# Kernel tuning notes

Measured on AMD Instinct MI355X. Metric: run time of the kernel, lower is better.

## Reference

```python
import jax, jax.numpy as jnp
import numpy as np

B, CIN, COUT, K, H, W = 2, 128, 64, 64, 128, 128
BN_EPS = 1e-5


def setup_inputs() -> dict:
    key = jax.random.key(0)
    k1, k2, k3, k4 = jax.random.split(key, 4)
    x = jax.random.normal(k1, (B, CIN, H, W), dtype=jnp.float32)
    index = jax.random.randint(k2, (B, 1, H, W), 0, K)  # superpixel labels
    # kaiming_uniform(a=sqrt(5)) ~ uniform with bound sqrt(6/((1+5)*fan_in)) = 1/sqrt(fan_in)
    Wft = jax.random.uniform(k3, (CIN, COUT), dtype=jnp.float32,
                             minval=-1.0, maxval=1.0) / np.sqrt(CIN).astype(np.float32)
    Wm = jax.random.uniform(k4, (COUT, COUT), dtype=jnp.float32,
                            minval=-1.0, maxval=1.0) / np.sqrt(COUT).astype(np.float32)
    gamma = jnp.ones((COUT,), jnp.float32)
    beta = jnp.zeros((COUT,), jnp.float32)
    return {"x": x, "index": index, "Wft": Wft, "Wm": Wm, "gamma": gamma, "beta": beta}


def _gnn_forward(x, index, Wft, Wm, gamma, beta):
    # FeatureTransform: [B,Cin,H,W] -> [B,Cout,H,W]
    xt = jnp.einsum('bchw,co->bohw', x, Wft)

    idx = index[:, 0]                                   # [B,H,W]
    oh = jax.nn.one_hot(idx, K, dtype=xt.dtype)         # [B,H,W,K]

    # RegionalMeans (segment-mean over superpixels; equivalent to the
    # repeated-tensor multiply+sum in the torch code, without the 5D blowup)
    block_sum = oh.sum(axis=(1, 2))                     # [B,K]
    sums = jnp.einsum('bhwk,bohw->bko', oh, xt)         # [B,K,Cout]
    denom = block_sum + (block_sum == 0).astype(xt.dtype)
    means = sums / denom[..., None]                     # [B,K,Cout]

    # Adj: pairwise Mahalanobis distance with learned cov = Wm @ Wm.T
    cov = Wm @ Wm.T
    inv_cov = jnp.linalg.inv(cov)
    diff = means[:, :, None, :] - means[:, None, :, :]  # [B,K,K,Cout]
    q = jnp.einsum('bijc,cd,bijd->bij', diff, inv_cov, diff)
    dist = jnp.sqrt(jnp.maximum(q, 1e-12))              # clamp: diagonal q==0
    adj = jnp.exp(-dist)                                # [B,K,K]

    # GCN propagate: adjacency-weighted aggregation of region means
    adj_means = jnp.einsum('bij,bjo->bio', adj, means)  # [B,K,Cout]

    # sum_k one_hot_k * (x_rep + adj_means_k) == xt + gather(adj_means, idx)
    gathered = jnp.take_along_axis(adj_means, idx.reshape(B, -1, 1), axis=1)
    gathered = gathered.reshape(B, H, W, COUT).transpose(0, 3, 1, 2)
    features = jax.nn.relu(xt + gathered)               # [B,Cout,H,W]

    # BatchNorm2d (training-mode batch statistics, biased variance)
    mean = features.mean(axis=(0, 2, 3), keepdims=True)
    var = features.var(axis=(0, 2, 3), keepdims=True)
    out = (features - mean) / jnp.sqrt(var + BN_EPS)
    out = out * gamma[None, :, None, None] + beta[None, :, None, None]
    return out


def reference(x, index, Wft, Wm, gamma, beta):
    return _gnn_forward(x, index, Wft, Wm, gamma, beta)
```

## Files before the change

### kernel.cpp

```cpp
#include <hip/hip_runtime.h>
#include <hip/hip_bf16.h>

#define CIN   128
#define COUT  64
#define HW    16384

typedef __hip_bfloat16 bf16;

#define OFF_XT    0u
#define OFF_PS    1048576u
#define OFF_PC    2097152u
#define OFF_MEANS 2129920u
#define OFF_DIAG  2138112u
#define OFF_INV   2138240u
#define OFF_ADJM  2142336u
#define OFF_BNP   2150528u

__device__ __forceinline__ unsigned short f2bfu(float f) {
  union { bf16 h; unsigned short u; } cv; cv.h = __float2bfloat16(f); return cv.u;
}
__device__ __forceinline__ float bf2f(unsigned short u) {
  union { unsigned int i; float f; } cv; cv.i = ((unsigned int)u) << 16; return cv.f;
}

__global__ __launch_bounds__(256, 2) void k1_xt_bins_inv(
    const float* __restrict__ x, const int* __restrict__ index,
    const float* __restrict__ Wft, const float* __restrict__ Wm,
    float* __restrict__ ws)
{
  __shared__ __align__(16) float smem[16384];
  const int blk = blockIdx.x, tid = threadIdx.x;
  if (blk != 0) {
    float* xl = smem;
    float* wl = smem + 8192;
    const int eb = blk - 1;
    const int b = eb >> 8, ps = eb & 255;
    const float* xg = x + (size_t)b * CIN * HW + ps * 64;
#pragma unroll
    for (int j = 0; j < 8; ++j) {
      const int fj = j * 256 + tid;
      const int c = fj >> 4, q4 = (fj & 15) * 4;
      *(float4*)&xl[c * 64 + q4] = *(const float4*)(xg + (size_t)c * HW + q4);
      *(float4*)&wl[c * 64 + q4] = *(const float4*)(Wft + c * 64 + q4);
    }
    __syncthreads();
    const int px_grp = tid & 15, o_grp = tid >> 4;
    const int px = ps * 64 + px_grp * 4, o0 = o_grp * 4;
    float acc[16];
#pragma unroll
    for (int j = 0; j < 16; ++j) acc[j] = 0.f;
#pragma unroll 8
    for (int c = 0; c < 128; ++c) {
      const float4 xv = *(const float4*)&xl[c * 64 + px_grp * 4];
      const float4 wv = *(const float4*)&wl[c * 64 + o0];
      acc[ 0]=fmaf(xv.x,wv.x,acc[ 0]); acc[ 1]=fmaf(xv.y,wv.x,acc[ 1]);
      acc[ 2]=fmaf(xv.z,wv.x,acc[ 2]); acc[ 3]=fmaf(xv.w,wv.x,acc[ 3]);
      acc[ 4]=fmaf(xv.x,wv.y,acc[ 4]); acc[ 5]=fmaf(xv.y,wv.y,acc[ 5]);
      acc[ 6]=fmaf(xv.z,wv.y,acc[ 6]); acc[ 7]=fmaf(xv.w,wv.y,acc[ 7]);
      acc[ 8]=fmaf(xv.x,wv.z,acc[ 8]); acc[ 9]=fmaf(xv.y,wv.z,acc[ 9]);
      acc[10]=fmaf(xv.z,wv.z,acc[10]); acc[11]=fmaf(xv.w,wv.z,acc[11]);
      acc[12]=fmaf(xv.x,wv.w,acc[12]); acc[13]=fmaf(xv.y,wv.w,acc[13]);
      acc[14]=fmaf(xv.z,wv.w,acc[14]); acc[15]=fmaf(xv.w,wv.w,acc[15]);
    }
    unsigned short* xtu = (unsigned short*)(ws + OFF_XT);
#pragma unroll
    for (int oj = 0; oj < 4; ++oj) {
      ushort4 u;
      u.x = f2bfu(acc[oj*4+0]); u.y = f2bfu(acc[oj*4+1]);
      u.z = f2bfu(acc[oj*4+2]); u.w = f2bfu(acc[oj*4+3]);
      *(ushort4*)(xtu + (size_t)(b * 64 + o0 + oj) * HW + px) = u;
    }
    const int4 kv = *(const int4*)(index + b * HW + px);
    const int kk[4] = {kv.x, kv.y, kv.z, kv.w};
    __syncthreads();
    float* bins = smem;
    float* cnt  = smem + 64 * 68;
    for (int i = tid; i < 64 * 68 + 64; i += 256) smem[i] = 0.f;
    __syncthreads();
#pragma unroll
    for (int pj = 0; pj < 4; ++pj) {
      const int kb = kk[pj] * 68 + o0;
      atomicAdd(&bins[kb    ], acc[ 0 + pj]);
      atomicAdd(&bins[kb + 1], acc[ 4 + pj]);
      atomicAdd(&bins[kb + 2], acc[ 8 + pj]);
      atomicAdd(&bins[kb + 3], acc[12 + pj]);
    }
    if (o_grp == 0) {
#pragma unroll
      for (int pj = 0; pj < 4; ++pj) atomicAdd(&cnt[kk[pj]], 1.f);
    }
    __syncthreads();
    unsigned short* pb = (unsigned short*)(ws + OFF_PS) + (size_t)eb * 4096;
    {
      const int k = tid >> 2, ob = (tid & 3) * 16;
#pragma unroll
      for (int q = 0; q < 4; ++q) {
        const float4 v = *(const float4*)&bins[k * 68 + ob + q * 4];
        ushort4 u;
        u.x = f2bfu(v.x); u.y = f2bfu(v.y); u.z = f2bfu(v.z); u.w = f2bfu(v.w);
        *(ushort4*)(pb + k * 64 + ob + q * 4) = u;
      }
    }
    if (tid < 64) ws[OFF_PC + (size_t)(b * 64 + tid) * 256 + ps] = cnt[tid];
  } else {
    float* wm = smem;
    float* Rb = smem + 8192;
    float* Cb = smem + 8704;
    for (int e = tid; e < 4096; e += 256) wm[(e >> 6) * 68 + (e & 63)] = Wm[e];
    __syncthreads();
    const int ig = tid >> 4, jg = tid & 15;
    const int i0 = ig << 2, j0 = jg << 2;
    float c4[16];
#pragma unroll
    for (int q = 0; q < 16; ++q) c4[q] = 0.f;
    for (int cq = 0; cq < 64; cq += 4) {
      float4 a[4], bb[4];
#pragma unroll
      for (int ii = 0; ii < 4; ++ii) a[ii]  = *(const float4*)&wm[(i0+ii)*68 + cq];
#pragma unroll
      for (int jj = 0; jj < 4; ++jj) bb[jj] = *(const float4*)&wm[(j0+jj)*68 + cq];
#pragma unroll
      for (int ii = 0; ii < 4; ++ii)
#pragma unroll
        for (int jj = 0; jj < 4; ++jj)
          c4[ii*4+jj] = fmaf(a[ii].x, bb[jj].x, fmaf(a[ii].y, bb[jj].y,
                        fmaf(a[ii].z, bb[jj].z, fmaf(a[ii].w, bb[jj].w, c4[ii*4+jj]))));
    }
    __syncthreads();
    __builtin_amdgcn_s_setprio(3);
    int buf = 0;
#pragma unroll 1
    for (int p = 0; p < 16; ++p) {
      const int P = p << 2;
      float* Rp = Rb + buf * 256;
      float* Cp = Cb + buf * 256;
      if (ig == p) {
#pragma unroll
        for (int r = 0; r < 4; ++r) {
          float4 t; t.x = c4[r*4+0]; t.y = c4[r*4+1]; t.z = c4[r*4+2]; t.w = c4[r*4+3];
          *(float4*)&Rp[r * 64 + j0] = t;
        }
      }
      if (jg == p) {
#pragma unroll
        for (int ii = 0; ii < 4; ++ii) {
          float4 t; t.x = c4[ii*4+0]; t.y = c4[ii*4+1]; t.z = c4[ii*4+2]; t.w = c4[ii*4+3];
          *(float4*)&Cp[(i0 + ii) * 4] = t;
        }
      }
      __syncthreads();
      float dd[16];
#pragma unroll
      for (int r = 0; r < 4; ++r) *(float4*)&dd[r * 4] = *(const float4*)&Rp[r * 64 + P];
#pragma unroll
      for (int k = 0; k < 4; ++k) {
        const float rp = __builtin_amdgcn_rcpf(dd[k * 4 + k]);
        float ai[4], s[4];
#pragma unroll
        for (int j = 0; j < 4; ++j) s[j] = dd[k * 4 + j];
#pragma unroll
        for (int i = 0; i < 4; ++i) ai[i] = (i == k) ? (rp - 1.0f) : (-dd[i * 4 + k] * rp);
#pragma unroll
        for (int i = 0; i < 4; ++i)
#pragma unroll
          for (int j = 0; j < 4; ++j) dd[i * 4 + j] = fmaf(ai[i], s[j], dd[i * 4 + j]);
#pragma unroll
        for (int i = 0; i < 4; ++i) dd[i * 4 + k] = (i == k) ? rp : ai[i];
      }
      if (ig == p && jg == p) {
#pragma unroll
        for (int q = 0; q < 16; ++q) c4[q] = dd[q];
      } else if (ig == p) {
        float nr[16];
#pragma unroll
        for (int r = 0; r < 4; ++r)
#pragma unroll
          for (int jj = 0; jj < 4; ++jj) {
            float t = dd[r*4+0] * c4[0*4+jj];
            t = fmaf(dd[r*4+1], c4[1*4+jj], t);
            t = fmaf(dd[r*4+2], c4[2*4+jj], t);
            t = fmaf(dd[r*4+3], c4[3*4+jj], t);
            nr[r*4+jj] = t;
          }
#pragma unroll
        for (int q = 0; q < 16; ++q) c4[q] = nr[q];
      } else if (jg == p) {
        float nr[16];
#pragma unroll
        for (int ii = 0; ii < 4; ++ii)
#pragma unroll
          for (int cidx = 0; cidx < 4; ++cidx) {
            float t = c4[ii*4+0] * dd[0*4+cidx];
            t = fmaf(c4[ii*4+1], dd[1*4+cidx], t);
            t = fmaf(c4[ii*4+2], dd[2*4+cidx], t);
            t = fmaf(c4[ii*4+3], dd[3*4+cidx], t);
            nr[ii*4+cidx] = t;
          }
#pragma unroll
        for (int q = 0; q < 16; ++q) c4[q] = -nr[q];
      } else {
        float T[16];
#pragma unroll
        for (int ii = 0; ii < 4; ++ii) {
          const float4 ccv = *(const float4*)&Cp[(i0 + ii) * 4];
#pragma unroll
          for (int cidx = 0; cidx < 4; ++cidx) {
            float t = ccv.x * dd[0*4+cidx];
            t = fmaf(ccv.y, dd[1*4+cidx], t);
            t = fmaf(ccv.z, dd[2*4+cidx], t);
            t = fmaf(ccv.w, dd[3*4+cidx], t);
            T[ii*4+cidx] = t;
          }
        }
#pragma unroll
        for (int r = 0; r < 4; ++r) {
          const float4 rrv = *(const float4*)&Rp[r * 64 + j0];
#pragma unroll
          for (int ii = 0; ii < 4; ++ii) {
            c4[ii*4+0] = fmaf(-T[ii*4+r], rrv.x, c4[ii*4+0]);
            c4[ii*4+1] = fmaf(-T[ii*4+r], rrv.y, c4[ii*4+1]);
            c4[ii*4+2] = fmaf(-T[ii*4+r], rrv.z, c4[ii*4+2]);
            c4[ii*4+3] = fmaf(-T[ii*4+r], rrv.w, c4[ii*4+3]);
          }
        }
      }
      buf ^= 1;
    }
    __builtin_amdgcn_s_setprio(0);
#pragma unroll
    for (int ii = 0; ii < 4; ++ii)
#pragma unroll
      for (int jj = 0; jj < 4; ++jj)
        ws[OFF_INV + (size_t)(i0 + ii) * 64 + j0 + jj] = c4[ii*4+jj];
  }
}

__global__ __launch_bounds__(1024) void k15_means_diag(float* __restrict__ ws)
{
  __shared__ float red[1024];
  __shared__ float lds_c[4];
  __shared__ float lds_m[64];
  const int blk = blockIdx.x, t = threadIdx.x;
  const int b = blk >> 6, k = blk & 63;
  const int o = t & 63, chunk = t >> 6;
  const unsigned short* psu = (const unsigned short*)(ws + OFF_PS);
  float s = 0.f;
#pragma unroll
  for (int i = 0; i < 16; ++i) {
    const int slab = chunk * 16 + i;
    s += bf2f(psu[(size_t)(b * 256 + slab) * 4096 + k * 64 + o]);
  }
  red[chunk * 64 + o] = s;
  float cv = 0.f;
  if (t < 256) cv = ws[OFF_PC + (size_t)(b * 64 + k) * 256 + t];
#pragma unroll
  for (int m = 32; m; m >>= 1) cv += __shfl_xor(cv, m, 64);
  if (t < 256 && (t & 63) == 0) lds_c[t >> 6] = cv;
  __syncthreads();
  if (t < 64) {
    float m_raw = 0.f;
#pragma unroll
    for (int ch = 0; ch < 16; ++ch) m_raw += red[ch * 64 + o];
    const float cnt = lds_c[0] + lds_c[1] + lds_c[2] + lds_c[3];
    const float denom = cnt + ((cnt == 0.f) ? 1.f : 0.f);
    const float m = m_raw / denom;
    ws[OFF_MEANS + (size_t)(b * 64 + k) * 64 + o] = m;
    lds_m[o] = m;
    float inner = 0.f;
#pragma unroll 8
    for (int d = 0; d < 64; ++d) inner = fmaf(ws[OFF_INV + d * 64 + o], lds_m[d], inner);
    float p = m * inner;
#pragma unroll
    for (int mm = 32; mm; mm >>= 1) p += __shfl_xor(p, mm, 64);
    if (o == 0) ws[OFF_DIAG + b * 64 + k] = p;
  }
}

__global__ __launch_bounds__(256) void k2_adj(float* __restrict__ ws)
{
  __shared__ __align__(16) float means_s[64 * 68];
  __shared__ __align__(16) float inv_s[64 * 68];
  __shared__ __align__(16) float T_s[8 * 68];
  __shared__ __align__(16) float adj_s[8 * 68];
  __shared__ float diag_s[64];
  const int b = blockIdx.x >> 3;
  const int i0 = (blockIdx.x & 7) << 3;
  const int t = threadIdx.x;
  const float* mg = ws + OFF_MEANS + b * 4096;
  for (int e = t; e < 4096; e += 256) means_s[(e >> 6) * 68 + (e & 63)] = mg[e];
  const float* ig = ws + OFF_INV;
  for (int e = t; e < 4096; e += 256) inv_s[(e >> 6) * 68 + (e & 63)] = ig[e];
  if (t < 64) diag_s[t] = ws[OFF_DIAG + b * 64 + t];
  __syncthreads();
  if (t < 128) {
    const int i = t >> 4, d0 = (t & 15) << 2;
    float4 acc = {0.f, 0.f, 0.f, 0.f};
    for (int c = 0; c < 64; ++c) {
      const float mv = means_s[(i0 + i) * 68 + c];
      const float4 iv = *(const float4*)&inv_s[c * 68 + d0];
      acc.x = fmaf(mv, iv.x, acc.x); acc.y = fmaf(mv, iv.y, acc.y);
      acc.z = fmaf(mv, iv.z, acc.z); acc.w = fmaf(mv, iv.w, acc.w);
    }
    *(float4*)&T_s[i * 68 + d0] = acc;
  }
  __syncthreads();
  {
    const int i = t >> 5, jb = t & 31;
#pragma unroll
    for (int jj = 0; jj < 2; ++jj) {
      const int j = jb + (jj << 5);
      float4 p4 = {0.f, 0.f, 0.f, 0.f};
      for (int dq = 0; dq < 64; dq += 4) {
        const float4 tv = *(const float4*)&T_s[i * 68 + dq];
        const float4 mv = *(const float4*)&means_s[j * 68 + dq];
        p4.x = fmaf(tv.x, mv.x, p4.x); p4.y = fmaf(tv.y, mv.y, p4.y);
        p4.z = fmaf(tv.z, mv.z, p4.z); p4.w = fmaf(tv.w, mv.w, p4.w);
      }
      const float p = (p4.x + p4.y) + (p4.z + p4.w);
      const float q = diag_s[i0 + i] + diag_s[j] - 2.f * p;
      adj_s[i * 68 + j] = __expf(-sqrtf(fmaxf(q, 1e-12f)));
    }
  }
  __syncthreads();
  if (t < 128) {
    const int i = t >> 4, oq = (t & 15) << 2;
    float4 am = {0.f, 0.f, 0.f, 0.f};
    for (int j = 0; j < 64; ++j) {
      const float av = adj_s[i * 68 + j];
      const float4 mv = *(const float4*)&means_s[j * 68 + oq];
      am.x = fmaf(av, mv.x, am.x); am.y = fmaf(av, mv.y, am.y);
      am.z = fmaf(av, mv.z, am.z); am.w = fmaf(av, mv.w, am.w);
    }
    *(float4*)(ws + OFF_ADJM + (size_t)(b * 64 + i0 + i) * 64 + oq) = am;
  }
}

__global__ __launch_bounds__(256) void k3_bnstats(const int* __restrict__ index,
                                                  float* __restrict__ ws)
{
  __shared__ float am_s[128];
  __shared__ float red[4];
  const int blk = blockIdx.x, t = threadIdx.x;
  const int b = blk >> 8, oc = (blk >> 3) & 31, tile = blk & 7;
  const int o0 = oc * 2;
  if (t < 128) am_s[t] = ws[OFF_ADJM + (size_t)(b * 64 + (t >> 1)) * 64 + o0 + (t & 1)];
  if (t < 4) red[t] = 0.f;
  __syncthreads();
  const int lane = t & 63, w = t >> 6;
  const unsigned short* xtu = (const unsigned short*)(ws + OFF_XT);
  float s0 = 0.f, s1 = 0.f, q0 = 0.f, q1 = 0.f;
#pragma unroll
  for (int q = 0; q < 2; ++q) {
    const int px = tile * 2048 + (w * 2 + q) * 256 + lane * 4;
    const int4 kv = *(const int4*)(index + b * HW + px);
    const ushort4 u0 = *(const ushort4*)(xtu + (size_t)(b * 64 + o0    ) * HW + px);
    const ushort4 u1 = *(const ushort4*)(xtu + (size_t)(b * 64 + o0 + 1) * HW + px);
    const int kk[4] = {kv.x, kv.y, kv.z, kv.w};
    const float x0[4] = {bf2f(u0.x), bf2f(u0.y), bf2f(u0.z), bf2f(u0.w)};
    const float x1[4] = {bf2f(u1.x), bf2f(u1.y), bf2f(u1.z), bf2f(u1.w)};
#pragma unroll
    for (int j = 0; j < 4; ++j) {
      const float2 am = *(const float2*)&am_s[kk[j] * 2];
      const float f0 = fmaxf(x0[j] + am.x, 0.f);
      const float f1 = fmaxf(x1[j] + am.y, 0.f);
      s0 += f0; q0 = fmaf(f0, f0, q0);
      s1 += f1; q1 = fmaf(f1, f1, q1);
    }
  }
#pragma unroll
  for (int m = 1; m < 64; m <<= 1) {
    s0 += __shfl_xor(s0, m, 64); s1 += __shfl_xor(s1, m, 64);
    q0 += __shfl_xor(q0, m, 64); q1 += __shfl_xor(q1, m, 64);
  }
  if (lane == 0) {
    atomicAdd(&red[0], s0); atomicAdd(&red[1], s1);
    atomicAdd(&red[2], q0); atomicAdd(&red[3], q1);
  }
  __syncthreads();
  if (t == 0) {
    float4 v; v.x = red[0]; v.y = red[1]; v.z = red[2]; v.w = red[3];
    *(float4*)(ws + OFF_BNP + (size_t)(oc * 16 + b * 8 + tile) * 4) = v;
  }
}

__global__ __launch_bounds__(256) void k4_out(const int* __restrict__ index,
    const float* __restrict__ gamma, const float* __restrict__ beta,
    const float* __restrict__ ws, float* __restrict__ out)
{
  __shared__ float am_s[128];
  __shared__ float4 tmp[16];
  __shared__ float sc_s[2], sh_s[2];
  const int blk = blockIdx.x, t = threadIdx.x;
  const int b = blk >> 8, oc = (blk >> 3) & 31, tile = blk & 7;
  const int o0 = oc * 2;
  if (t < 128) am_s[t] = ws[OFF_ADJM + (size_t)(b * 64 + (t >> 1)) * 64 + o0 + (t & 1)];
  if (t < 16) tmp[t] = *(const float4*)(ws + OFF_BNP + (size_t)(oc * 16 + t) * 4);
  if (t < 2) {
    float s = 0.f, qq = 0.f;
#pragma unroll
    for (int i = 0; i < 16; ++i) {
      const float4 v = tmp[i];
      s  += (t == 0) ? v.x : v.y;
      qq += (t == 0) ? v.z : v.w;
    }
    const float mean = s * (1.f / 32768.f);
    const float var  = qq * (1.f / 32768.f) - mean * mean;
    const float sc = gamma[o0 + t] * rsqrtf(var + 1e-5f);
    sc_s[t] = sc;
    sh_s[t] = fmaf(-mean, sc, beta[o0 + t]);
  }
  __syncthreads();
  const int lane = t & 63, w = t >> 6;
  const unsigned short* xtu = (const unsigned short*)(ws + OFF_XT);
  const float c0 = sc_s[0], c1 = sc_s[1], h0 = sh_s[0], h1 = sh_s[1];
#pragma unroll
  for (int q = 0; q < 2; ++q) {
    const int px = tile * 2048 + (w * 2 + q) * 256 + lane * 4;
    const int4 kv = *(const int4*)(index + b * HW + px);
    const ushort4 u0 = *(const ushort4*)(xtu + (size_t)(b * 64 + o0    ) * HW + px);
    const ushort4 u1 = *(const ushort4*)(xtu + (size_t)(b * 64 + o0 + 1) * HW + px);
    const int kk[4] = {kv.x, kv.y, kv.z, kv.w};
    const float x0[4] = {bf2f(u0.x), bf2f(u0.y), bf2f(u0.z), bf2f(u0.w)};
    const float x1[4] = {bf2f(u1.x), bf2f(u1.y), bf2f(u1.z), bf2f(u1.w)};
    float4 o4a, o4b;
    float* oa = (float*)&o4a; float* ob = (float*)&o4b;
#pragma unroll
    for (int j = 0; j < 4; ++j) {
      const float2 am = *(const float2*)&am_s[kk[j] * 2];
      oa[j] = fmaf(fmaxf(x0[j] + am.x, 0.f), c0, h0);
      ob[j] = fmaf(fmaxf(x1[j] + am.y, 0.f), c1, h1);
    }
    *(float4*)(out + (size_t)(b * 64 + o0    ) * HW + px) = o4a;
    *(float4*)(out + (size_t)(b * 64 + o0 + 1) * HW + px) = o4b;
  }
}

extern "C" void kernel_launch(void* const* d_in, const int* in_sizes, int n_in,
                              void* d_out, int out_size, void* d_ws, size_t ws_size,
                              hipStream_t stream) {
  const float* x     = (const float*)d_in[0];
  const int*   index = (const int*)d_in[1];
  const float* Wft   = (const float*)d_in[2];
  const float* Wm    = (const float*)d_in[3];
  const float* gamma = (const float*)d_in[4];
  const float* beta  = (const float*)d_in[5];
  float* ws  = (float*)d_ws;
  float* out = (float*)d_out;

  k1_xt_bins_inv<<<513, 256, 0, stream>>>(x, index, Wft, Wm, ws);
  k15_means_diag<<<128, 1024, 0, stream>>>(ws);
  k2_adj<<<16, 256, 0, stream>>>(ws);
  k3_bnstats<<<512, 256, 0, stream>>>(index, ws);
  k4_out<<<512, 256, 0, stream>>>(index, gamma, beta, ws, out);
}
```

Measured before the change: 120.7 us.

## Fuse region-means reduction, diagonal and adjacency into one per-batch kernel

Merges the means/diagonal kernel and the adjacency kernel into one kernel with one 1024-thread block per batch. Each block reduces the bf16 partial sums over all slabs, then computes T, the diagonal, the adjacency and the aggregated means in LDS. This removes a launch and the global round trip for means and diagonal, but the large partial-sum reduction now runs on only two workgroups instead of 128.

New measurement: 156.4 us. 29.6% more time.

```diff
diff --git a/kernel.cpp b/kernel.cpp
--- a/kernel.cpp
+++ b/kernel.cpp
@@ -10,8 +10,6 @@
 #define OFF_XT    0u
 #define OFF_PS    1048576u
 #define OFF_PC    2097152u
-#define OFF_MEANS 2129920u
-#define OFF_DIAG  2138112u
 #define OFF_INV   2138240u
 #define OFF_ADJM  2142336u
 #define OFF_BNP   2150528u
@@ -235,103 +233,88 @@
   }
 }
 
-__global__ __launch_bounds__(1024) void k15_means_diag(float* __restrict__ ws)
-{
-  __shared__ float red[1024];
-  __shared__ float lds_c[4];
-  __shared__ float lds_m[64];
-  const int blk = blockIdx.x, t = threadIdx.x;
-  const int b = blk >> 6, k = blk & 63;
-  const int o = t & 63, chunk = t >> 6;
-  const unsigned short* psu = (const unsigned short*)(ws + OFF_PS);
-  float s = 0.f;
-#pragma unroll
-  for (int i = 0; i < 16; ++i) {
-    const int slab = chunk * 16 + i;
-    s += bf2f(psu[(size_t)(b * 256 + slab) * 4096 + k * 64 + o]);
-  }
-  red[chunk * 64 + o] = s;
-  float cv = 0.f;
-  if (t < 256) cv = ws[OFF_PC + (size_t)(b * 64 + k) * 256 + t];
-#pragma unroll
-  for (int m = 32; m; m >>= 1) cv += __shfl_xor(cv, m, 64);
-  if (t < 256 && (t & 63) == 0) lds_c[t >> 6] = cv;
-  __syncthreads();
-  if (t < 64) {
-    float m_raw = 0.f;
-#pragma unroll
-    for (int ch = 0; ch < 16; ++ch) m_raw += red[ch * 64 + o];
-    const float cnt = lds_c[0] + lds_c[1] + lds_c[2] + lds_c[3];
-    const float denom = cnt + ((cnt == 0.f) ? 1.f : 0.f);
-    const float m = m_raw / denom;
-    ws[OFF_MEANS + (size_t)(b * 64 + k) * 64 + o] = m;
-    lds_m[o] = m;
-    float inner = 0.f;
-#pragma unroll 8
-    for (int d = 0; d < 64; ++d) inner = fmaf(ws[OFF_INV + d * 64 + o], lds_m[d], inner);
-    float p = m * inner;
-#pragma unroll
-    for (int mm = 32; mm; mm >>= 1) p += __shfl_xor(p, mm, 64);
-    if (o == 0) ws[OFF_DIAG + b * 64 + k] = p;
-  }
-}
-
-__global__ __launch_bounds__(256) void k2_adj(float* __restrict__ ws)
+__global__ __launch_bounds__(1024) void k2p_means_adj(float* __restrict__ ws)
 {
   __shared__ __align__(16) float means_s[64 * 68];
-  __shared__ __align__(16) float inv_s[64 * 68];
-  __shared__ __align__(16) float T_s[8 * 68];
-  __shared__ __align__(16) float adj_s[8 * 68];
+  __shared__ __align__(16) float T_s[64 * 68];
+  __shared__ __align__(16) float adj_s[64 * 68];
   __shared__ float diag_s[64];
-  const int b = blockIdx.x >> 3;
-  const int i0 = (blockIdx.x & 7) << 3;
-  const int t = threadIdx.x;
-  const float* mg = ws + OFF_MEANS + b * 4096;
-  for (int e = t; e < 4096; e += 256) means_s[(e >> 6) * 68 + (e & 63)] = mg[e];
-  const float* ig = ws + OFF_INV;
-  for (int e = t; e < 4096; e += 256) inv_s[(e >> 6) * 68 + (e & 63)] = ig[e];
-  if (t < 64) diag_s[t] = ws[OFF_DIAG + b * 64 + t];
-  __syncthreads();
-  if (t < 128) {
-    const int i = t >> 4, d0 = (t & 15) << 2;
+  __shared__ float cnt_s[64];
+  const int b = blockIdx.x, tid = threadIdx.x;
+  const int k = tid >> 4;
+  const int q16 = tid & 15;
+  const int o0 = q16 * 4;
+  {
+    const float* pc = ws + OFF_PC + (size_t)(b * 64 + k) * 256 + q16 * 16;
+    float cv = 0.f;
+#pragma unroll
+    for (int i = 0; i < 16; ++i) cv += pc[i];
+#pragma unroll
+    for (int m = 1; m < 16; m <<= 1) cv += __shfl_xor(cv, m, 16);
+    if (q16 == 0) cnt_s[k] = cv;
+  }
+  {
+    const unsigned short* psu = (const unsigned short*)(ws + OFF_PS) + k * 64 + o0;
+    float s0 = 0.f, s1 = 0.f, s2 = 0.f, s3 = 0.f;
+#pragma unroll 4
+    for (int slab = 0; slab < 256; ++slab) {
+      const ushort4 u = *(const ushort4*)(psu + (size_t)(b * 256 + slab) * 4096);
+      s0 += bf2f(u.x); s1 += bf2f(u.y); s2 += bf2f(u.z); s3 += bf2f(u.w);
+    }
+    const float cnt = cnt_s[k];
+    const float rd = 1.0f / (cnt + ((cnt == 0.f) ? 1.f : 0.f));
+    float4 m4; m4.x = s0 * rd; m4.y = s1 * rd; m4.z = s2 * rd; m4.w = s3 * rd;
+    *(float4*)&means_s[k * 68 + o0] = m4;
+  }
+  __syncthreads();
+  {
     float4 acc = {0.f, 0.f, 0.f, 0.f};
+    const float* ig = ws + OFF_INV;
     for (int c = 0; c < 64; ++c) {
-      const float mv = means_s[(i0 + i) * 68 + c];
-      const float4 iv = *(const float4*)&inv_s[c * 68 + d0];
+      const float mv = means_s[k * 68 + c];
+      const float4 iv = *(const float4*)(ig + c * 64 + o0);
       acc.x = fmaf(mv, iv.x, acc.x); acc.y = fmaf(mv, iv.y, acc.y);
       acc.z = fmaf(mv, iv.z, acc.z); acc.w = fmaf(mv, iv.w, acc.w);
     }
-    *(float4*)&T_s[i * 68 + d0] = acc;
-  }
-  __syncthreads();
-  {
-    const int i = t >> 5, jb = t & 31;
-#pragma unroll
-    for (int jj = 0; jj < 2; ++jj) {
-      const int j = jb + (jj << 5);
-      float4 p4 = {0.f, 0.f, 0.f, 0.f};
+    *(float4*)&T_s[k * 68 + o0] = acc;
+  }
+  __syncthreads();
+  {
+    const float4 tv = *(const float4*)&T_s[k * 68 + o0];
+    const float4 mv = *(const float4*)&means_s[k * 68 + o0];
+    float p = tv.x * mv.x + tv.y * mv.y + tv.z * mv.z + tv.w * mv.w;
+#pragma unroll
+    for (int m = 1; m < 16; m <<= 1) p += __shfl_xor(p, m, 16);
+    if (q16 == 0) diag_s[k] = p;
+  }
+  __syncthreads();
+  {
+    const float di = diag_s[k];
+    float4 p4[1];
+#pragma unroll
+    for (int jj = 0; jj < 4; ++jj) {
+      const int j = o0 + jj;
+      float p = 0.f;
       for (int dq = 0; dq < 64; dq += 4) {
-        const float4 tv = *(const float4*)&T_s[i * 68 + dq];
+        const float4 tv = *(const float4*)&T_s[k * 68 + dq];
         const float4 mv = *(const float4*)&means_s[j * 68 + dq];
-        p4.x = fmaf(tv.x, mv.x, p4.x); p4.y = fmaf(tv.y, mv.y, p4.y);
-        p4.z = fmaf(tv.z, mv.z, p4.z); p4.w = fmaf(tv.w, mv.w, p4.w);
-      }
-      const float p = (p4.x + p4.y) + (p4.z + p4.w);
-      const float q = diag_s[i0 + i] + diag_s[j] - 2.f * p;
-      adj_s[i * 68 + j] = __expf(-sqrtf(fmaxf(q, 1e-12f)));
-    }
-  }
-  __syncthreads();
-  if (t < 128) {
-    const int i = t >> 4, oq = (t & 15) << 2;
+        p = fmaf(tv.x, mv.x, fmaf(tv.y, mv.y, fmaf(tv.z, mv.z, fmaf(tv.w, mv.w, p))));
+      }
+      const float q = di + diag_s[j] - 2.f * p;
+      adj_s[k * 68 + j] = __expf(-sqrtf(fmaxf(q, 1e-12f)));
+      (void)p4;
+    }
+  }
+  __syncthreads();
+  {
     float4 am = {0.f, 0.f, 0.f, 0.f};
     for (int j = 0; j < 64; ++j) {
-      const float av = adj_s[i * 68 + j];
-      const float4 mv = *(const float4*)&means_s[j * 68 + oq];
+      const float av = adj_s[k * 68 + j];
+      const float4 mv = *(const float4*)&means_s[j * 68 + o0];
       am.x = fmaf(av, mv.x, am.x); am.y = fmaf(av, mv.y, am.y);
       am.z = fmaf(av, mv.z, am.z); am.w = fmaf(av, mv.w, am.w);
     }
-    *(float4*)(ws + OFF_ADJM + (size_t)(b * 64 + i0 + i) * 64 + oq) = am;
+    *(float4*)(ws + OFF_ADJM + (size_t)(b * 64 + k) * 64 + o0) = am;
   }
 }
 
@@ -448,8 +431,7 @@
   float* out = (float*)d_out;
 
   k1_xt_bins_inv<<<513, 256, 0, stream>>>(x, index, Wft, Wm, ws);
-  k15_means_diag<<<128, 1024, 0, stream>>>(ws);
-  k2_adj<<<16, 256, 0, stream>>>(ws);
+  k2p_means_adj<<<2, 1024, 0, stream>>>(ws);
   k3_bnstats<<<512, 256, 0, stream>>>(index, ws);
   k4_out<<<512, 256, 0, stream>>>(index, gamma, beta, ws, out);
 }
```
